# Kernel optimization log

Measured on AMD Instinct MI355X. Metric: run time of the kernel, lower is better.

Reference implementation:

```python
import jax, jax.numpy as jnp
import numpy as np

R_MAX = 32
S_MAX = 2
DIM_OUT = 128
N_R = 2 * R_MAX + 2            # 66 bins for rel_pos / rel_token
N_S = 2 * S_MAX + 2            # 6 bins for rel_chain
DIM_IN = 2 * N_R + 1 + N_S     # 139 packed feature dim: [rel_pos|rel_token|mask|rel_chain]


def setup_inputs() -> dict:
    key = jax.random.key(0)
    # LinearNoBias weight, torch convention: y = x @ W.T, W: (dim_out, dim_in)
    W = jax.random.normal(key, (DIM_OUT, DIM_IN), dtype=jnp.float32) * 0.02
    return {"batch_size": 1, "seq_len": 1024, "W": W}


def reference(batch_size, seq_len, W):
    # token_idx = arange(seq_len) (no chain breaks => complex_chain_break_indices is None)
    tok = jnp.arange(seq_len)
    diff = tok[:, None] - tok[None, :]                      # (n, n) = i - j
    # d_token = clip(diff + r_max, 0, 2*r_max); onehot bins = arange(66).
    # argmin |v - arange(66)| == v for integer v in [0, 64], so the one-hot
    # index is exactly the clipped value (embedding-gather form of the
    # original onehot + dense matmul).
    bucket = jnp.clip(diff + R_MAX, 0, 2 * R_MAX)           # (n, n) int
    # d_res is constant r_max -> one-hot index r_max in rel_pos block.
    # mask_same_entity is constant 1.
    # d_chain is constant 2*s_max+1 -> one-hot index 2*s_max+1 in rel_chain block.
    W_pos = W[:, :N_R]                                      # (dim_out, 66)
    W_token = W[:, N_R:2 * N_R]                             # (dim_out, 66)
    w_mask = W[:, 2 * N_R]                                  # (dim_out,)
    W_chain = W[:, 2 * N_R + 1:]                            # (dim_out, 6)
    const = W_pos[:, R_MAX] + w_mask + W_chain[:, 2 * S_MAX + 1]  # (dim_out,)
    out = jnp.take(W_token.T, bucket, axis=0) + const       # (n, n, dim_out)
    return jnp.broadcast_to(out[None], (batch_size, seq_len, seq_len, DIM_OUT))
```

## Files before the change

### kernel.cpp

```cpp
#include <hip/hip_runtime.h>

#define R_MAX 32
#define DIM_OUT 128
#define N_R 66
#define DIM_IN 139

typedef float f32x4 __attribute__((ext_vector_type(4)));

__global__ __launch_bounds__(256) void rpe_kernel(const int* __restrict__ p_seq,
                                                  const float* __restrict__ W,
                                                  f32x4* __restrict__ out,
                                                  unsigned long long n_rows) {
    const unsigned seq = (unsigned)*p_seq;
    const unsigned tid = threadIdx.x;
    const unsigned lane = tid & 31;
    const float* w0 = W + (size_t)(lane * 4) * DIM_IN;

    float cst[4];
    f32x4 vhi, vlo;
    #pragma unroll
    for (int k = 0; k < 4; ++k) {
        const float* w = w0 + (size_t)k * DIM_IN;
        cst[k] = (w[R_MAX] + w[2 * N_R]) + w[DIM_IN - 1];
        vhi[k] = w[N_R + 2 * R_MAX] + cst[k];
        vlo[k] = w[N_R + 0] + cst[k];
    }

    const unsigned n_irows = (unsigned)(n_rows / seq);
    const unsigned CPR = 2;
    const unsigned total_chunks = n_irows * CPR;

    for (unsigned chunk = blockIdx.x; chunk < total_chunks; chunk += gridDim.x) {
        const unsigned irow = chunk / CPR;
        const unsigned half = chunk - irow * CPR;
        const int i = (int)(irow % seq);
        const int j0 = (int)((half * seq) / CPR);
        const int j1 = (int)(((half + 1) * seq) / CPR);

        int e1 = i - 31; e1 = e1 < j0 ? j0 : (e1 > j1 ? j1 : e1);
        int e2 = i + 32; e2 = e2 < j0 ? j0 : (e2 > j1 ? j1 : e2);

        f32x4* __restrict__ base = out + (size_t)irow * seq * (DIM_OUT / 4);

        for (int f = j0 * 32 + (int)tid; f < e1 * 32; f += 256)
            __builtin_nontemporal_store(vhi, base + f);

        for (int f = e1 * 32 + (int)tid; f < e2 * 32; f += 256) {
            const int j = f >> 5;
            const int b = i - j + R_MAX;
            f32x4 v;
            v[0] = w0[0 * DIM_IN + N_R + b] + cst[0];
            v[1] = w0[1 * DIM_IN + N_R + b] + cst[1];
            v[2] = w0[2 * DIM_IN + N_R + b] + cst[2];
            v[3] = w0[3 * DIM_IN + N_R + b] + cst[3];
            __builtin_nontemporal_store(v, base + f);
        }

        for (int f = e2 * 32 + (int)tid; f < j1 * 32; f += 256)
            __builtin_nontemporal_store(vlo, base + f);
    }
}

extern "C" void kernel_launch(void* const* d_in, const int* in_sizes, int n_in,
                              void* d_out, int out_size, void* d_ws, size_t ws_size,
                              hipStream_t stream) {
    const int* p_seq = (const int*)d_in[1];
    const float* W = (const float*)d_in[2];
    f32x4* out = (f32x4*)d_out;

    const unsigned long long n_rows = (unsigned long long)out_size / DIM_OUT;

    rpe_kernel<<<2048, 256, 0, stream>>>(p_seq, W, out, n_rows);
}
```

Baseline: 105.8 us.

## Assign whole row groups per block, unroll fill stores, shrink grid

Each block now handles groups of four full output rows instead of half-rows, with a reduced grid of 256 blocks. The constant fill loops are manually unrolled by four so more stores are in flight per thread. The aim is to cut per-chunk index overhead and raise store throughput for this write-bound kernel. The risk is fewer waves on the device, which could leave compute units idle and lower achieved bandwidth.

New measurement: 110.1 us. 4.0% more time.

```diff
diff --git a/kernel.cpp b/kernel.cpp
--- a/kernel.cpp
+++ b/kernel.cpp
@@ -4,6 +4,7 @@
 #define DIM_OUT 128
 #define N_R 66
 #define DIM_IN 139
+#define IROWS_PER_BLOCK 4
 
 typedef float f32x4 __attribute__((ext_vector_type(4)));
 
@@ -27,37 +28,50 @@
     }
 
     const unsigned n_irows = (unsigned)(n_rows / seq);
-    const unsigned CPR = 2;
-    const unsigned total_chunks = n_irows * CPR;
+    const unsigned n_groups = (n_irows + IROWS_PER_BLOCK - 1) / IROWS_PER_BLOCK;
 
-    for (unsigned chunk = blockIdx.x; chunk < total_chunks; chunk += gridDim.x) {
-        const unsigned irow = chunk / CPR;
-        const unsigned half = chunk - irow * CPR;
-        const int i = (int)(irow % seq);
-        const int j0 = (int)((half * seq) / CPR);
-        const int j1 = (int)(((half + 1) * seq) / CPR);
+    for (unsigned g = blockIdx.x; g < n_groups; g += gridDim.x) {
+        const unsigned r_end = min((g + 1) * IROWS_PER_BLOCK, n_irows);
+        for (unsigned irow = g * IROWS_PER_BLOCK; irow < r_end; ++irow) {
+            const int i = (int)(irow % seq);
 
-        int e1 = i - 31; e1 = e1 < j0 ? j0 : (e1 > j1 ? j1 : e1);
-        int e2 = i + 32; e2 = e2 < j0 ? j0 : (e2 > j1 ? j1 : e2);
+            int e1 = i - 31; e1 = e1 < 0 ? 0 : (e1 > (int)seq ? (int)seq : e1);
+            int e2 = i + 32; e2 = e2 < 0 ? 0 : (e2 > (int)seq ? (int)seq : e2);
 
-        f32x4* __restrict__ base = out + (size_t)irow * seq * (DIM_OUT / 4);
+            f32x4* __restrict__ base = out + (size_t)irow * seq * (DIM_OUT / 4);
 
-        for (int f = j0 * 32 + (int)tid; f < e1 * 32; f += 256)
-            __builtin_nontemporal_store(vhi, base + f);
+            int f = (int)tid, end = e1 * 32;
+            for (; f + 768 < end; f += 1024) {
+                __builtin_nontemporal_store(vhi, base + f);
+                __builtin_nontemporal_store(vhi, base + f + 256);
+                __builtin_nontemporal_store(vhi, base + f + 512);
+                __builtin_nontemporal_store(vhi, base + f + 768);
+            }
+            for (; f < end; f += 256)
+                __builtin_nontemporal_store(vhi, base + f);
 
-        for (int f = e1 * 32 + (int)tid; f < e2 * 32; f += 256) {
-            const int j = f >> 5;
-            const int b = i - j + R_MAX;
-            f32x4 v;
-            v[0] = w0[0 * DIM_IN + N_R + b] + cst[0];
-            v[1] = w0[1 * DIM_IN + N_R + b] + cst[1];
-            v[2] = w0[2 * DIM_IN + N_R + b] + cst[2];
-            v[3] = w0[3 * DIM_IN + N_R + b] + cst[3];
-            __builtin_nontemporal_store(v, base + f);
+            f = e1 * 32 + (int)tid; end = e2 * 32;
+            for (; f < end; f += 256) {
+                const int j = f >> 5;
+                const int b = i - j + R_MAX;
+                f32x4 v;
+                v[0] = w0[0 * DIM_IN + N_R + b] + cst[0];
+                v[1] = w0[1 * DIM_IN + N_R + b] + cst[1];
+                v[2] = w0[2 * DIM_IN + N_R + b] + cst[2];
+                v[3] = w0[3 * DIM_IN + N_R + b] + cst[3];
+                __builtin_nontemporal_store(v, base + f);
+            }
+
+            f = e2 * 32 + (int)tid; end = (int)seq * 32;
+            for (; f + 768 < end; f += 1024) {
+                __builtin_nontemporal_store(vlo, base + f);
+                __builtin_nontemporal_store(vlo, base + f + 256);
+                __builtin_nontemporal_store(vlo, base + f + 512);
+                __builtin_nontemporal_store(vlo, base + f + 768);
+            }
+            for (; f < end; f += 256)
+                __builtin_nontemporal_store(vlo, base + f);
         }
-
-        for (int f = e2 * 32 + (int)tid; f < j1 * 32; f += 256)
-            __builtin_nontemporal_store(vlo, base + f);
     }
 }
 
@@ -70,5 +84,5 @@
 
     const unsigned long long n_rows = (unsigned long long)out_size / DIM_OUT;
 
-    rpe_kernel<<<2048, 256, 0, stream>>>(p_seq, W, out, n_rows);
+    rpe_kernel<<<256, 256, 0, stream>>>(p_seq, W, out, n_rows);
 }
```
